# Kernel tuning notes

Measured on AMD Instinct MI355X. Metric: run time of the kernel, lower is better.

Reference implementation:

```python
import jax, jax.numpy as jnp
import numpy as np

B, T, D = 2, 1024, 2048
H, HKV, DH = 16, 4, 128
G = H // HKV  # GQA groups
F = 5632
ROPE_THETA = 10000.0
EPS = 1e-6


def _rope_tables(t, dh, theta):
    inv = 1.0 / (theta ** (np.arange(0, dh, 2, dtype=np.float32) / dh))  # [dh//2]
    ang = np.outer(np.arange(t, dtype=np.float32), inv)                  # [T, dh//2]
    return jnp.asarray(np.cos(ang)), jnp.asarray(np.sin(ang))


def setup_inputs() -> dict:
    key = jax.random.key(0)
    ks = jax.random.split(key, 9)
    s = 0.02
    cos, sin = _rope_tables(T, DH, ROPE_THETA)
    return {
        "x": jax.random.normal(ks[0], (B, T, D), jnp.float32),
        "freqs_cos": cos,
        "freqs_sin": sin,
        "w_norm1": jnp.ones((D,), jnp.float32),
        "w_norm2": jnp.ones((D,), jnp.float32),
        "wq": jax.random.normal(ks[1], (D, H * DH), jnp.float32) * s,
        "wk": jax.random.normal(ks[2], (D, HKV * DH), jnp.float32) * s,
        "wv": jax.random.normal(ks[3], (D, HKV * DH), jnp.float32) * s,
        "wo": jax.random.normal(ks[4], (D, D), jnp.float32) * s,
        "w1": jax.random.normal(ks[5], (D, F), jnp.float32) * s,
        "w2": jax.random.normal(ks[6], (F, D), jnp.float32) * s,
        "w3": jax.random.normal(ks[7], (D, F), jnp.float32) * s,
    }


def _rmsnorm(x, w):
    var = jnp.mean(jnp.square(x), axis=-1, keepdims=True)
    return x * jax.lax.rsqrt(var + EPS) * w


def _apply_rope(x, cos, sin):
    # x: [B, T, nH, DH]; cos/sin: [T, DH//2]
    xr = x.reshape(*x.shape[:-1], DH // 2, 2)
    x0, x1 = xr[..., 0], xr[..., 1]
    c = cos[None, :, None, :]
    s = sin[None, :, None, :]
    o0 = x0 * c - x1 * s
    o1 = x0 * s + x1 * c
    return jnp.stack([o0, o1], axis=-1).reshape(x.shape)


def reference(x, freqs_cos, freqs_sin, w_norm1, w_norm2, wq, wk, wv, wo, w1, w2, w3):
    residual = x
    xn = _rmsnorm(x, w_norm1)
    q = (xn @ wq).reshape(B, T, H, DH)
    k = (xn @ wk).reshape(B, T, HKV, DH)
    v = (xn @ wv).reshape(B, T, HKV, DH)
    q = _apply_rope(q, freqs_cos, freqs_sin)
    k = _apply_rope(k, freqs_cos, freqs_sin)
    # grouped heads: q -> [B, HKV, G, T, DH]; k,v -> [B, HKV, T, DH]
    q = q.transpose(0, 2, 1, 3).reshape(B, HKV, G, T, DH)
    k = k.transpose(0, 2, 1, 3)
    v = v.transpose(0, 2, 1, 3)
    scale = DH ** -0.5
    scores = jnp.einsum("bkgtd,bksd->bkgts", q, k) * scale  # [B,HKV,G,T,T]
    causal = jnp.tril(jnp.ones((T, T), dtype=bool))
    scores = jnp.where(causal, scores, -jnp.inf)
    attn = jax.nn.softmax(scores, axis=-1)
    out = jnp.einsum("bkgts,bksd->bkgtd", attn, v)  # [B,HKV,G,T,DH]
    out = out.reshape(B, H, T, DH).transpose(0, 2, 1, 3).reshape(B, T, D)
    x = residual + out @ wo
    h = _rmsnorm(x, w_norm2)
    ffn = (jax.nn.silu(h @ w1) * (h @ w3)) @ w2
    return x + ffn
```

## Files before the change

kernel.cpp:

```cpp
#include <hip/hip_runtime.h>
#include <hip/hip_bf16.h>
#include <math.h>

typedef __hip_bfloat16 bf16;
typedef __attribute__((ext_vector_type(8))) short bf16x8;
typedef __attribute__((ext_vector_type(4))) float f32x4;

__device__ __forceinline__ float b2f(bf16 v) { return __bfloat162float(v); }
__device__ __forceinline__ bf16  f2b(float v) { return __float2bfloat16(v); }

constexpr int Bc = 2, Tc = 1024, Dc = 2048, Hc = 16, HKVc = 4, DHc = 128, Fc = 5632;
constexpr int Mr = Bc * Tc;
constexpr int Nqkv = Hc * DHc + 2 * HKVc * DHc;

__device__ __forceinline__ void g2l16(void* lds, const void* g) {
  __builtin_amdgcn_global_load_lds(
      (const __attribute__((address_space(1))) unsigned int*)g,
      (__attribute__((address_space(3))) unsigned int*)lds, 16, 0, 0);
}

__global__ __launch_bounds__(256) void tcast_k(const float* __restrict__ src,
                                               bf16* __restrict__ dst,
                                               int N, int K) {
  __shared__ bf16 tile[64][68];
  const int t = threadIdx.x;
  const int n0 = blockIdx.x * 64, k0 = blockIdx.y * 64;
#pragma unroll
  for (int it = 0; it < 4; ++it) {
    const int kl = it * 16 + (t >> 4);
    const int nl = (t & 15) * 4;
    float4 v = *reinterpret_cast<const float4*>(src + (size_t)(k0 + kl) * N + n0 + nl);
    tile[kl][nl]     = f2b(v.x);
    tile[kl][nl + 1] = f2b(v.y);
    tile[kl][nl + 2] = f2b(v.z);
    tile[kl][nl + 3] = f2b(v.w);
  }
  __syncthreads();
  union { uint4 u; bf16 h[8]; } o;
#pragma unroll
  for (int it = 0; it < 2; ++it) {
    const int nl = it * 32 + (t >> 3);
    const int kl = (t & 7) * 8;
#pragma unroll
    for (int j = 0; j < 8; ++j) o.h[j] = tile[kl + j][nl];
    *reinterpret_cast<uint4*>(dst + (size_t)(n0 + nl) * K + k0 + kl) = o.u;
  }
}

__global__ __launch_bounds__(256) void tcast_ffn(const float* __restrict__ src,
                                                 bf16* __restrict__ dst,
                                                 int off) {
  __shared__ bf16 tile[64][68];
  const int t = threadIdx.x;
  const int n0 = blockIdx.x * 64, k0 = blockIdx.y * 64;
#pragma unroll
  for (int it = 0; it < 4; ++it) {
    const int kl = it * 16 + (t >> 4);
    const int nl = (t & 15) * 4;
    float4 v = *reinterpret_cast<const float4*>(src + (size_t)(k0 + kl) * Fc + n0 + nl);
    tile[kl][nl]     = f2b(v.x);
    tile[kl][nl + 1] = f2b(v.y);
    tile[kl][nl + 2] = f2b(v.z);
    tile[kl][nl + 3] = f2b(v.w);
  }
  __syncthreads();
  union { uint4 u; bf16 h[8]; } o;
#pragma unroll
  for (int it = 0; it < 2; ++it) {
    const int nl = it * 32 + (t >> 3);
    const int kl = (t & 7) * 8;
#pragma unroll
    for (int j = 0; j < 8; ++j) o.h[j] = tile[kl + j][nl];
    const int n = n0 + nl;
    const int r = ((n >> 4) << 5) + (n & 15) + off;
    *reinterpret_cast<uint4*>(dst + (size_t)r * Dc + k0 + kl) = o.u;
  }
}

__global__ __launch_bounds__(256) void rmsnorm_k(const float* __restrict__ x,
                                                 const float* __restrict__ w,
                                                 bf16* __restrict__ out) {
  const size_t rbase = (size_t)blockIdx.x * Dc;
  float ss = 0.f;
  for (int i = threadIdx.x; i < Dc; i += 256) {
    float v = x[rbase + i];
    ss += v * v;
  }
#pragma unroll
  for (int off = 32; off > 0; off >>= 1) ss += __shfl_down(ss, off, 64);
  __shared__ float red[4];
  const int lane = threadIdx.x & 63, wid = threadIdx.x >> 6;
  if (lane == 0) red[wid] = ss;
  __syncthreads();
  const float scale = rsqrtf((red[0] + red[1] + red[2] + red[3]) / (float)Dc + 1e-6f);
  for (int i = threadIdx.x; i < Dc; i += 256)
    out[rbase + i] = f2b(x[rbase + i] * scale * w[i]);
}

__global__ __launch_bounds__(256) void reduce4_rms(const float* __restrict__ P,
                                                   const float* __restrict__ x,
                                                   const float* __restrict__ w,
                                                   float* __restrict__ xat,
                                                   bf16* __restrict__ hb) {
  constexpr size_t PS = (size_t)Mr * Dc;
  const size_t base4 = (size_t)blockIdx.x * (Dc / 4);
  const int t = threadIdx.x;
  float4 v[2];
  float ss = 0.f;
#pragma unroll
  for (int j = 0; j < 2; ++j) {
    const size_t c4 = base4 + t + j * 256;
    float4 a = reinterpret_cast<const float4*>(x)[c4];
#pragma unroll
    for (int z = 0; z < 4; ++z) {
      float4 q = reinterpret_cast<const float4*>(P + z * PS)[c4];
      a.x += q.x; a.y += q.y; a.z += q.z; a.w += q.w;
    }
    reinterpret_cast<float4*>(xat)[c4] = a;
    ss += a.x * a.x + a.y * a.y + a.z * a.z + a.w * a.w;
    v[j] = a;
  }
#pragma unroll
  for (int off = 32; off > 0; off >>= 1) ss += __shfl_down(ss, off, 64);
  __shared__ float red[4];
  const int lane = t & 63, wid = t >> 6;
  if (lane == 0) red[wid] = ss;
  __syncthreads();
  const float scale = rsqrtf((red[0] + red[1] + red[2] + red[3]) / (float)Dc + 1e-6f);
  bf16* hrow = hb + (size_t)blockIdx.x * Dc;
#pragma unroll
  for (int j = 0; j < 2; ++j) {
    const int c = (t + j * 256) * 4;
    hrow[c]     = f2b(v[j].x * scale * w[c]);
    hrow[c + 1] = f2b(v[j].y * scale * w[c + 1]);
    hrow[c + 2] = f2b(v[j].z * scale * w[c + 2]);
    hrow[c + 3] = f2b(v[j].w * scale * w[c + 3]);
  }
}

__global__ __launch_bounds__(256) void reduce4_add(const float* __restrict__ P,
                                                   const float* __restrict__ res,
                                                   float* __restrict__ out) {
  constexpr size_t PS = (size_t)Mr * Dc;
  const size_t c4 = (size_t)blockIdx.x * 256 + threadIdx.x;
  float4 a = reinterpret_cast<const float4*>(res)[c4];
#pragma unroll
  for (int z = 0; z < 4; ++z) {
    float4 q = reinterpret_cast<const float4*>(P + z * PS)[c4];
    a.x += q.x; a.y += q.y; a.z += q.z; a.w += q.w;
  }
  reinterpret_cast<float4*>(out)[c4] = a;
}

template <int K>
__global__ __launch_bounds__(512, 2) void ffn_gemm256(const bf16* __restrict__ A,
                                                      const bf16* __restrict__ B,
                                                      bf16* __restrict__ act) {
  constexpr int NT = K / 64;
  constexpr int NIT = NT / 2;
  __shared__ bf16 As[2 * 256 * 64];
  __shared__ bf16 Bs[3 * 256 * 64];
  const int tid = threadIdx.x;
  const int lane = tid & 63, wv = tid >> 6;
  const int wr = wv >> 2, wc = wv & 3;
  const int fr = lane & 15, quad = lane >> 4;
  const int swz = fr & 7;
  const int bm = blockIdx.y * 256;
  const int bn = blockIdx.x * 256;
  const int lrow = tid >> 3;
  const int scol = ((tid & 7) ^ (lrow & 7)) * 8;
  const size_t rstep = (size_t)64 * K;

  auto stageA = [&](int t, int half) {
    const int buf = (t & 1) * 16384;
    const bf16* g = A + (size_t)(bm + half * 128 + lrow) * K + t * 64 + scol;
    bf16* d = As + buf + half * 8192 + (size_t)tid * 8;
    g2l16(d, g);
    g2l16(d + 4096, g + rstep);
  };
  auto stageB = [&](int t, int half, int buf) {
    const bf16* g = B + (size_t)(bn + half * 128 + lrow) * K + t * 64 + scol;
    bf16* d = Bs + buf * 16384 + half * 8192 + (size_t)tid * 8;
    g2l16(d, g);
    g2l16(d + 4096, g + rstep);
  };

  f32x4 acc[8][4] = {};
  const int u0 = (quad ^ swz) * 8;

  stageA(0, 0); stageA(0, 1);
  stageB(0, 0, 0); stageB(0, 1, 0);
  stageB(1, 0, 1); stageB(1, 1, 1);
  asm volatile("s_waitcnt vmcnt(4)" ::: "memory");
  __builtin_amdgcn_s_barrier();

  int rb0 = 0, rb1 = 1, sb = 2;
  for (int it = 0; it < NIT; ++it) {
    const int t1 = 2 * it + 1;
#pragma unroll
    for (int j = 0; j < 8; ++j) {
      const int bufT = (j < 4) ? 0 : 16384;
      const int bufB = ((j < 4) ? rb0 : rb1) * 16384;
      const int qr4 = ((j & 3) >> 1) * 4, qc2 = ((j & 3) & 1) * 2;
      bf16x8 af[4][2], bv[2][2];
      const bf16* Ab = As + bufT + (size_t)(wr * 128 + fr) * 64;
      const bf16* Bb = Bs + bufB + (size_t)(wc * 64 + fr) * 64;
#pragma unroll
      for (int ii = 0; ii < 4; ++ii) {
        af[ii][0] = *reinterpret_cast<const bf16x8*>(Ab + (qr4 + ii) * 1024 + u0);
        af[ii][1] = *reinterpret_cast<const bf16x8*>(Ab + (qr4 + ii) * 1024 + (u0 ^ 32));
      }
#pragma unroll
      for (int jj = 0; jj < 2; ++jj) {
        bv[jj][0] = *reinterpret_cast<const bf16x8*>(Bb + (qc2 + jj) * 1024 + u0);
        bv[jj][1] = *reinterpret_cast<const bf16x8*>(Bb + (qc2 + jj) * 1024 + (u0 ^ 32));
      }
      if (j == 0)      stageA(t1, 0);
      else if (j == 1) stageA(t1, 1);
      else if (j == 2) { if (2 * it + 2 < NT) stageB(2 * it + 2, 0, sb); }
      else if (j == 3) { if (2 * it + 2 < NT) stageB(2 * it + 2, 1, sb); }
      else if (j == 4) { if (2 * it + 2 < NT) stageA(2 * it + 2, 0); }
      else if (j == 5) { if (2 * it + 2 < NT) stageA(2 * it + 2, 1); }
      else if (j == 6) { if (2 * it + 3 < NT) stageB(2 * it + 3, 0, rb0); }
      else             { if (2 * it + 3 < NT) stageB(2 * it + 3, 1, rb0); }
      __builtin_amdgcn_s_barrier();
      asm volatile("s_waitcnt lgkmcnt(0)" ::: "memory");
      __builtin_amdgcn_sched_barrier(0);
      __builtin_amdgcn_s_setprio(1);
#pragma unroll
      for (int ii = 0; ii < 4; ++ii)
#pragma unroll
        for (int jj = 0; jj < 2; ++jj) {
          acc[qr4 + ii][qc2 + jj] = __builtin_amdgcn_mfma_f32_16x16x32_bf16(
              af[ii][0], bv[jj][0], acc[qr4 + ii][qc2 + jj], 0, 0, 0);
          acc[qr4 + ii][qc2 + jj] = __builtin_amdgcn_mfma_f32_16x16x32_bf16(
              af[ii][1], bv[jj][1], acc[qr4 + ii][qc2 + jj], 0, 0, 0);
        }
      __builtin_amdgcn_s_setprio(0);
      if (j == 3) {
        if (2 * it + 2 < NT) asm volatile("s_waitcnt vmcnt(4)" ::: "memory");
        else                 asm volatile("s_waitcnt vmcnt(0)" ::: "memory");
      } else if (j == 7) {
        if (2 * it + 3 < NT)      asm volatile("s_waitcnt vmcnt(4)" ::: "memory");
        else if (2 * it + 2 < NT) asm volatile("s_waitcnt vmcnt(0)" ::: "memory");
      }
      __builtin_amdgcn_s_barrier();
    }
    const int nrb0 = sb; sb = rb1; rb1 = rb0; rb0 = nrb0;
  }

  const int er = quad * 4, ec = lane & 15;
#pragma unroll
  for (int i = 0; i < 8; ++i) {
    const int row = bm + wr * 128 + i * 16 + er;
#pragma unroll
    for (int jp = 0; jp < 2; ++jp) {
      const f32x4 g = acc[i][2 * jp], u = acc[i][2 * jp + 1];
      const int f = blockIdx.x * 128 + wc * 32 + jp * 16 + ec;
#pragma unroll
      for (int r = 0; r < 4; ++r) {
        const float sg = g[r] / (1.f + __expf(-g[r]));
        act[(size_t)(row + r) * Fc + f] = f2b(sg * u[r]);
      }
    }
  }
}

template <int KFULL, int KSUB>
__global__ __launch_bounds__(512, 2) void gemm256sk(const bf16* __restrict__ A,
                                                    const bf16* __restrict__ Bt,
                                                    float* __restrict__ Part,
                                                    int N) {
  constexpr int NT = KSUB / 64;
  constexpr int NIT = NT / 2;
  __shared__ bf16 As[2 * 256 * 64];
  __shared__ bf16 Bs[3 * 256 * 64];
  const int tid = threadIdx.x;
  const int lane = tid & 63, wv = tid >> 6;
  const int wr = wv >> 2, wc = wv & 3;
  const int fr = lane & 15, quad = lane >> 4;
  const int swz = fr & 7;
  const int bm = blockIdx.y * 256;
  const int bn = blockIdx.x * 256;
  const int kbase = blockIdx.z * KSUB;
  const int lrow = tid >> 3;
  const int scol = ((tid & 7) ^ (lrow & 7)) * 8;
  const size_t rstep = (size_t)64 * KFULL;

  auto stageA = [&](int t, int half) {
    const int buf = (t & 1) * 16384;
    const bf16* g = A + (size_t)(bm + half * 128 + lrow) * KFULL + kbase + t * 64 + scol;
    bf16* d = As + buf + half * 8192 + (size_t)tid * 8;
    g2l16(d, g);
    g2l16(d + 4096, g + rstep);
  };
  auto stageB = [&](int t, int half, int buf) {
    const bf16* g = Bt + (size_t)(bn + half * 128 + lrow) * KFULL + kbase + t * 64 + scol;
    bf16* d = Bs + buf * 16384 + half * 8192 + (size_t)tid * 8;
    g2l16(d, g);
    g2l16(d + 4096, g + rstep);
  };

  f32x4 acc[8][4] = {};
  const int u0 = (quad ^ swz) * 8;

  stageA(0, 0); stageA(0, 1);
  stageB(0, 0, 0); stageB(0, 1, 0);
  stageB(1, 0, 1); stageB(1, 1, 1);
  asm volatile("s_waitcnt vmcnt(4)" ::: "memory");
  __builtin_amdgcn_s_barrier();

  int rb0 = 0, rb1 = 1, sb = 2;
  for (int it = 0; it < NIT; ++it) {
    const int t1 = 2 * it + 1;
#pragma unroll
    for (int j = 0; j < 8; ++j) {
      const int bufT = (j < 4) ? 0 : 16384;
      const int bufB = ((j < 4) ? rb0 : rb1) * 16384;
      const int qr4 = ((j & 3) >> 1) * 4, qc2 = ((j & 3) & 1) * 2;
      bf16x8 af[4][2], bv[2][2];
      const bf16* Ab = As + bufT + (size_t)(wr * 128 + fr) * 64;
      const bf16* Bb = Bs + bufB + (size_t)(wc * 64 + fr) * 64;
#pragma unroll
      for (int ii = 0; ii < 4; ++ii) {
        af[ii][0] = *reinterpret_cast<const bf16x8*>(Ab + (qr4 + ii) * 1024 + u0);
        af[ii][1] = *reinterpret_cast<const bf16x8*>(Ab + (qr4 + ii) * 1024 + (u0 ^ 32));
      }
#pragma unroll
      for (int jj = 0; jj < 2; ++jj) {
        bv[jj][0] = *reinterpret_cast<const bf16x8*>(Bb + (qc2 + jj) * 1024 + u0);
        bv[jj][1] = *reinterpret_cast<const bf16x8*>(Bb + (qc2 + jj) * 1024 + (u0 ^ 32));
      }
      if (j == 0)      stageA(t1, 0);
      else if (j == 1) stageA(t1, 1);
      else if (j == 2) { if (2 * it + 2 < NT) stageB(2 * it + 2, 0, sb); }
      else if (j == 3) { if (2 * it + 2 < NT) stageB(2 * it + 2, 1, sb); }
      else if (j == 4) { if (2 * it + 2 < NT) stageA(2 * it + 2, 0); }
      else if (j == 5) { if (2 * it + 2 < NT) stageA(2 * it + 2, 1); }
      else if (j == 6) { if (2 * it + 3 < NT) stageB(2 * it + 3, 0, rb0); }
      else             { if (2 * it + 3 < NT) stageB(2 * it + 3, 1, rb0); }
      __builtin_amdgcn_s_barrier();
      asm volatile("s_waitcnt lgkmcnt(0)" ::: "memory");
      __builtin_amdgcn_sched_barrier(0);
      __builtin_amdgcn_s_setprio(1);
#pragma unroll
      for (int ii = 0; ii < 4; ++ii)
#pragma unroll
        for (int jj = 0; jj < 2; ++jj) {
          acc[qr4 + ii][qc2 + jj] = __builtin_amdgcn_mfma_f32_16x16x32_bf16(
              af[ii][0], bv[jj][0], acc[qr4 + ii][qc2 + jj], 0, 0, 0);
          acc[qr4 + ii][qc2 + jj] = __builtin_amdgcn_mfma_f32_16x16x32_bf16(
              af[ii][1], bv[jj][1], acc[qr4 + ii][qc2 + jj], 0, 0, 0);
        }
      __builtin_amdgcn_s_setprio(0);
      if (j == 3) {
        if (2 * it + 2 < NT) asm volatile("s_waitcnt vmcnt(4)" ::: "memory");
        else                 asm volatile("s_waitcnt vmcnt(0)" ::: "memory");
      } else if (j == 7) {
        if (2 * it + 3 < NT)      asm volatile("s_waitcnt vmcnt(4)" ::: "memory");
        else if (2 * it + 2 < NT) asm volatile("s_waitcnt vmcnt(0)" ::: "memory");
      }
      __builtin_amdgcn_s_barrier();
    }
    const int nrb0 = sb; sb = rb1; rb1 = rb0; rb0 = nrb0;
  }

  float* P = Part + (size_t)blockIdx.z * ((size_t)Mr * N);
  const int er = quad * 4, ec = lane & 15;
#pragma unroll
  for (int i = 0; i < 8; ++i) {
    const int row = bm + wr * 128 + i * 16 + er;
#pragma unroll
    for (int jc = 0; jc < 4; ++jc) {
      const int col = bn + wc * 64 + jc * 16 + ec;
#pragma unroll
      for (int r = 0; r < 4; ++r)
        P[(size_t)(row + r) * N + col] = acc[i][jc][r];
    }
  }
}

__global__ __launch_bounds__(256) void repack_k(const float* __restrict__ P,
                                                const float* __restrict__ cosb,
                                                const float* __restrict__ sinb,
                                                bf16* __restrict__ Qr,
                                                bf16* __restrict__ Kr,
                                                bf16* __restrict__ Vt) {
  constexpr size_t PS = (size_t)Mr * Nqkv;
  const int bt = blockIdx.x;
  const int b = bt >> 10, tp = bt & (Tc - 1);
  const int t0 = threadIdx.x;
  const float* r0 = P + (size_t)bt * Nqkv;
  const float* r1 = r0 + PS;
#pragma unroll
  for (int k = 0; k < 4; ++k) {
    int p2 = k * 256 + t0;
    int hh = p2 >> 6, i = p2 & 63;
    float c = cosb[tp * 64 + i], sn = sinb[tp * 64 + i];
    float2 v0 = *reinterpret_cast<const float2*>(r0 + hh * 128 + 2 * i);
    float2 v1 = *reinterpret_cast<const float2*>(r1 + hh * 128 + 2 * i);
    float x0 = v0.x + v1.x, x1 = v0.y + v1.y;
    bf16* dst = Qr + ((size_t)(b * Hc + hh) * Tc + tp) * DHc + 2 * i;
    dst[0] = f2b(x0 * c - x1 * sn);
    dst[1] = f2b(x0 * sn + x1 * c);
  }
  {
    int hh = t0 >> 6, i = t0 & 63;
    float c = cosb[tp * 64 + i], sn = sinb[tp * 64 + i];
    float2 v0 = *reinterpret_cast<const float2*>(r0 + 2048 + hh * 128 + 2 * i);
    float2 v1 = *reinterpret_cast<const float2*>(r1 + 2048 + hh * 128 + 2 * i);
    float x0 = v0.x + v1.x, x1 = v0.y + v1.y;
    bf16* dst = Kr + ((size_t)(b * HKVc + hh) * Tc + tp) * DHc + 2 * i;
    dst[0] = f2b(x0 * c - x1 * sn);
    dst[1] = f2b(x0 * sn + x1 * c);
  }
#pragma unroll
  for (int k = 0; k < 2; ++k) {
    int e = k * 256 + t0;
    int kvh = e >> 7, dd = e & 127;
    Vt[((size_t)(b * HKVc + kvh) * DHc + dd) * Tc + tp] = f2b(r0[2560 + e] + r1[2560 + e]);
  }
}

__global__ __launch_bounds__(256) void fattn(const bf16* __restrict__ Qr,
                                             const bf16* __restrict__ Kr,
                                             const bf16* __restrict__ Vt,
                                             bf16* __restrict__ ao) {
  __shared__ __align__(16) bf16 Ks[64 * 136];
  __shared__ __align__(16) bf16 Vts[128 * 72];
  __shared__ __align__(16) bf16 Ps[4][16 * 72];
  const int idx = blockIdx.x;
  const int r = idx & 15;
  const int qt = (r & 1) ? (15 - (r >> 1)) : (r >> 1);
  const int h = (idx >> 4) & 15;
  const int b = idx >> 8;
  const int kv = h >> 2;
  const int t = threadIdx.x, lane = t & 63, wv = t >> 6;
  const int fr = lane & 15, quad = lane >> 4;

  const bf16* Qbase = Qr + ((size_t)(b * Hc + h) * Tc + qt * 64) * DHc;
  const bf16* Kbase = Kr + (size_t)(b * HKVc + kv) * Tc * DHc;
  const bf16* Vbase = Vt + (size_t)(b * HKVc + kv) * DHc * Tc;

  bf16x8 qf[4];
#pragma unroll
  for (int c = 0; c < 4; ++c)
    qf[c] = *reinterpret_cast<const bf16x8*>(Qbase + (size_t)(wv * 16 + fr) * DHc + c * 32 + quad * 8);

  float m[4], l[4];
  f32x4 o[8] = {};
#pragma unroll
  for (int r2 = 0; r2 < 4; ++r2) { m[r2] = -3.0e38f; l[r2] = 0.f; }

  for (int kt = 0; kt <= qt; ++kt) {
    __syncthreads();
    {
      const bf16* src = Kbase + (size_t)kt * 64 * DHc;
#pragma unroll
      for (int i2 = 0; i2 < 4; ++i2) {
        int flat = i2 * 256 + t;
        int row = flat >> 4, c16 = flat & 15;
        uint4 v = *reinterpret_cast<const uint4*>(src + (size_t)row * DHc + c16 * 8);
        *reinterpret_cast<uint4*>(&Ks[row * 136 + c16 * 8]) = v;
      }
#pragma unroll
      for (int i2 = 0; i2 < 4; ++i2) {
        int flat = i2 * 256 + t;
        int row = flat >> 3, c8 = flat & 7;
        uint4 v = *reinterpret_cast<const uint4*>(Vbase + (size_t)row * Tc + kt * 64 + c8 * 8);
        *reinterpret_cast<uint4*>(&Vts[row * 72 + c8 * 8]) = v;
      }
    }
    __syncthreads();
    f32x4 s[4];
#pragma unroll
    for (int cb = 0; cb < 4; ++cb) {
      f32x4 acc = {};
#pragma unroll
      for (int kc = 0; kc < 4; ++kc) {
        bf16x8 kf = *reinterpret_cast<const bf16x8*>(&Ks[(cb * 16 + fr) * 136 + kc * 32 + quad * 8]);
        acc = __builtin_amdgcn_mfma_f32_16x16x32_bf16(qf[kc], kf, acc, 0, 0, 0);
      }
      s[cb] = acc * 0.08838834764831845f;
    }
    if (kt == qt) {
#pragma unroll
      for (int cb = 0; cb < 4; ++cb)
#pragma unroll
        for (int r2 = 0; r2 < 4; ++r2) {
          int key = cb * 16 + fr;
          int qg = wv * 16 + quad * 4 + r2;
          if (key > qg) s[cb][r2] = -3.0e38f;
        }
    }
    float tm[4], ts[4];
#pragma unroll
    for (int r2 = 0; r2 < 4; ++r2)
      tm[r2] = fmaxf(fmaxf(s[0][r2], s[1][r2]), fmaxf(s[2][r2], s[3][r2]));
#pragma unroll
    for (int off = 1; off < 16; off <<= 1)
#pragma unroll
      for (int r2 = 0; r2 < 4; ++r2)
        tm[r2] = fmaxf(tm[r2], __shfl_xor(tm[r2], off, 64));
    float al[4];
#pragma unroll
    for (int r2 = 0; r2 < 4; ++r2) {
      float mn = fmaxf(m[r2], tm[r2]);
      al[r2] = __expf(m[r2] - mn);
      m[r2] = mn;
      ts[r2] = 0.f;
    }
#pragma unroll
    for (int cb = 0; cb < 4; ++cb)
#pragma unroll
      for (int r2 = 0; r2 < 4; ++r2) {
        float e = __expf(s[cb][r2] - m[r2]);
        s[cb][r2] = e;
        ts[r2] += e;
      }
#pragma unroll
    for (int off = 1; off < 16; off <<= 1)
#pragma unroll
      for (int r2 = 0; r2 < 4; ++r2)
        ts[r2] += __shfl_xor(ts[r2], off, 64);
#pragma unroll
    for (int r2 = 0; r2 < 4; ++r2) l[r2] = l[r2] * al[r2] + ts[r2];
#pragma unroll
    for (int db = 0; db < 8; ++db)
#pragma unroll
      for (int r2 = 0; r2 < 4; ++r2) o[db][r2] *= al[r2];
    bf16* pw = Ps[wv];
#pragma unroll
    for (int cb = 0; cb < 4; ++cb)
#pragma unroll
      for (int r2 = 0; r2 < 4; ++r2)
        pw[(quad * 4 + r2) * 72 + cb * 16 + fr] = f2b(s[cb][r2]);
    bf16x8 pa[2];
    pa[0] = *reinterpret_cast<const bf16x8*>(&pw[fr * 72 + quad * 8]);
    pa[1] = *reinterpret_cast<const bf16x8*>(&pw[fr * 72 + 32 + quad * 8]);
#pragma unroll
    for (int db = 0; db < 8; ++db) {
      bf16x8 v0 = *reinterpret_cast<const bf16x8*>(&Vts[(db * 16 + fr) * 72 + quad * 8]);
      bf16x8 v1 = *reinterpret_cast<const bf16x8*>(&Vts[(db * 16 + fr) * 72 + 32 + quad * 8]);
      o[db] = __builtin_amdgcn_mfma_f32_16x16x32_bf16(pa[0], v0, o[db], 0, 0, 0);
      o[db] = __builtin_amdgcn_mfma_f32_16x16x32_bf16(pa[1], v1, o[db], 0, 0, 0);
    }
  }
#pragma unroll
  for (int r2 = 0; r2 < 4; ++r2) {
    float inv = 1.f / l[r2];
    int qg = qt * 64 + wv * 16 + quad * 4 + r2;
    bf16* orow = ao + (size_t)(b * Tc + qg) * Dc + h * DHc;
#pragma unroll
    for (int db = 0; db < 8; ++db)
      orow[db * 16 + fr] = f2b(o[db][r2] * inv);
  }
}

extern "C" void kernel_launch(void* const* d_in, const int* in_sizes, int n_in,
                              void* d_out, int out_size, void* d_ws, size_t ws_size,
                              hipStream_t stream) {
  const float* x    = (const float*)d_in[0];
  const float* fcos = (const float*)d_in[1];
  const float* fsin = (const float*)d_in[2];
  const float* wn1  = (const float*)d_in[3];
  const float* wn2  = (const float*)d_in[4];
  const float* wq   = (const float*)d_in[5];
  const float* wk   = (const float*)d_in[6];
  const float* wv   = (const float*)d_in[7];
  const float* wo   = (const float*)d_in[8];
  const float* w1   = (const float*)d_in[9];
  const float* w2   = (const float*)d_in[10];
  const float* w3   = (const float*)d_in[11];

  char* p = (char*)d_ws;
  bf16* wqkv_t = (bf16*)p;                 p += (size_t)Nqkv * Dc * 2;
  float* xat   = (float*)d_ws;
  bf16* wo_t = (bf16*)p;                   p += (size_t)Dc * Dc * 2;
  bf16* w13t = (bf16*)p;                   p += (size_t)2 * Fc * Dc * 2;
  bf16* w2t  = w13t;
  bf16* xn   = (bf16*)p;                   p += (size_t)Mr * Dc * 2;
  bf16* ao   = (bf16*)p;                   p += (size_t)Mr * Dc * 2;
  bf16* act  = (bf16*)p;                   p += (size_t)Mr * Fc * 2;
  float* Pbuf = (float*)p;                 p += (size_t)4 * Mr * Dc * 4;
  bf16* hb = xn;
  bf16* Qr = act;
  bf16* Kr = act + (size_t)Mr * Hc * DHc;
  bf16* Vtb = Kr + (size_t)Mr * HKVc * DHc;

  const dim3 blk(256);
  tcast_k<<<dim3(32, 32), blk, 0, stream>>>(wq, wqkv_t, 2048, 2048);
  tcast_k<<<dim3(8, 32), blk, 0, stream>>>(wk, wqkv_t + (size_t)2048 * 2048, 512, 2048);
  tcast_k<<<dim3(8, 32), blk, 0, stream>>>(wv, wqkv_t + (size_t)2560 * 2048, 512, 2048);
  tcast_k<<<dim3(32, 32), blk, 0, stream>>>(wo, wo_t, 2048, 2048);
  tcast_ffn<<<dim3(88, 32), blk, 0, stream>>>(w1, w13t, 0);
  tcast_ffn<<<dim3(88, 32), blk, 0, stream>>>(w3, w13t, 16);

  rmsnorm_k<<<Mr, blk, 0, stream>>>(x, wn1, xn);
  gemm256sk<Dc, 1024><<<dim3(Nqkv / 256, Mr / 256, 2), dim3(512), 0, stream>>>(xn, wqkv_t, Pbuf, Nqkv);
  repack_k<<<Mr, blk, 0, stream>>>(Pbuf, fcos, fsin, Qr, Kr, Vtb);
  fattn<<<Bc * Hc * 16, blk, 0, stream>>>(Qr, Kr, Vtb, ao);
  gemm256sk<Dc, 512><<<dim3(Dc / 256, Mr / 256, 4), dim3(512), 0, stream>>>(ao, wo_t, Pbuf, Dc);
  reduce4_rms<<<Mr, blk, 0, stream>>>(Pbuf, x, wn2, xat, hb);
  ffn_gemm256<Dc><<<dim3(2 * Fc / 256, Mr / 256), dim3(512), 0, stream>>>(hb, w13t, act);
  tcast_k<<<dim3(32, 88), blk, 0, stream>>>(w2, w2t, 2048, 5632);
  gemm256sk<Fc, 1408><<<dim3(Dc / 256, Mr / 256, 4), dim3(512), 0, stream>>>(act, w2t, Pbuf, Dc);
  reduce4_add<<<Mr * Dc / 1024, blk, 0, stream>>>(Pbuf, xat, (float*)d_out);
}
```

Baseline: 564.3 us.

## Double-buffer K/V tiles in flash attention with async LDS loads and XOR swizzle

The attention kernel now prefetches the next K and V tiles into a second LDS buffer using global_load_lds while MFMAs run on the current tile. The LDS layout changes from a padded layout to an XOR-swizzled one to avoid bank conflicts, and s_setprio raises wave priority around the MFMA sections. This aims to hide global-load latency and cut one barrier per iteration. In exchange it doubles LDS use for K/V, which may lower occupancy, and it depends on the async loads having landed by the single trailing barrier.

```diff
diff --git a/kernel.cpp b/kernel.cpp
--- a/kernel.cpp
+++ b/kernel.cpp
@@ -426,8 +426,8 @@
                                              const bf16* __restrict__ Kr,
                                              const bf16* __restrict__ Vt,
                                              bf16* __restrict__ ao) {
-  __shared__ __align__(16) bf16 Ks[64 * 136];
-  __shared__ __align__(16) bf16 Vts[128 * 72];
+  __shared__ __align__(16) bf16 Ks[2][64 * 128];
+  __shared__ __align__(16) bf16 Vts[2][128 * 64];
   __shared__ __align__(16) bf16 Ps[4][16 * 72];
   const int idx = blockIdx.x;
   const int r = idx & 15;
@@ -442,6 +442,24 @@
   const bf16* Kbase = Kr + (size_t)(b * HKVc + kv) * Tc * DHc;
   const bf16* Vbase = Vt + (size_t)(b * HKVc + kv) * DHc * Tc;
 
+  auto stageK = [&](int kt, int buf) {
+    const bf16* src = Kbase + (size_t)kt * 64 * DHc;
+#pragma unroll
+    for (int rr = 0; rr < 4; ++rr) {
+      const int row = rr * 16 + (t >> 4);
+      const int cS = (t & 15) ^ (row & 7);
+      g2l16(&Ks[buf][rr * 2048 + t * 8], src + row * DHc + cS * 8);
+    }
+  };
+  auto stageV = [&](int kt, int buf) {
+#pragma unroll
+    for (int rr = 0; rr < 4; ++rr) {
+      const int row = rr * 32 + (t >> 3);
+      const int cS = (t & 7) ^ (row & 7);
+      g2l16(&Vts[buf][rr * 2048 + t * 8], Vbase + (size_t)row * Tc + kt * 64 + cS * 8);
+    }
+  };
+
   bf16x8 qf[4];
 #pragma unroll
   for (int c = 0; c < 4; ++c)
@@ -452,37 +470,28 @@
 #pragma unroll
   for (int r2 = 0; r2 < 4; ++r2) { m[r2] = -3.0e38f; l[r2] = 0.f; }
 
+  stageK(0, 0);
+  stageV(0, 0);
+  __syncthreads();
+  int buf = 0;
+
   for (int kt = 0; kt <= qt; ++kt) {
-    __syncthreads();
-    {
-      const bf16* src = Kbase + (size_t)kt * 64 * DHc;
-#pragma unroll
-      for (int i2 = 0; i2 < 4; ++i2) {
-        int flat = i2 * 256 + t;
-        int row = flat >> 4, c16 = flat & 15;
-        uint4 v = *reinterpret_cast<const uint4*>(src + (size_t)row * DHc + c16 * 8);
-        *reinterpret_cast<uint4*>(&Ks[row * 136 + c16 * 8]) = v;
-      }
-#pragma unroll
-      for (int i2 = 0; i2 < 4; ++i2) {
-        int flat = i2 * 256 + t;
-        int row = flat >> 3, c8 = flat & 7;
-        uint4 v = *reinterpret_cast<const uint4*>(Vbase + (size_t)row * Tc + kt * 64 + c8 * 8);
-        *reinterpret_cast<uint4*>(&Vts[row * 72 + c8 * 8]) = v;
-      }
-    }
-    __syncthreads();
+    if (kt < qt) { stageK(kt + 1, buf ^ 1); stageV(kt + 1, buf ^ 1); }
+    const int sw = fr & 7;
     f32x4 s[4];
+    __builtin_amdgcn_s_setprio(1);
 #pragma unroll
     for (int cb = 0; cb < 4; ++cb) {
       f32x4 acc = {};
 #pragma unroll
       for (int kc = 0; kc < 4; ++kc) {
-        bf16x8 kf = *reinterpret_cast<const bf16x8*>(&Ks[(cb * 16 + fr) * 136 + kc * 32 + quad * 8]);
+        bf16x8 kf = *reinterpret_cast<const bf16x8*>(
+            &Ks[buf][(cb * 16 + fr) * 128 + (((kc << 2) + quad) ^ sw) * 8]);
         acc = __builtin_amdgcn_mfma_f32_16x16x32_bf16(qf[kc], kf, acc, 0, 0, 0);
       }
       s[cb] = acc * 0.08838834764831845f;
     }
+    __builtin_amdgcn_s_setprio(0);
     if (kt == qt) {
 #pragma unroll
       for (int cb = 0; cb < 4; ++cb)
@@ -538,13 +547,19 @@
     bf16x8 pa[2];
     pa[0] = *reinterpret_cast<const bf16x8*>(&pw[fr * 72 + quad * 8]);
     pa[1] = *reinterpret_cast<const bf16x8*>(&pw[fr * 72 + 32 + quad * 8]);
+    __builtin_amdgcn_s_setprio(1);
 #pragma unroll
     for (int db = 0; db < 8; ++db) {
-      bf16x8 v0 = *reinterpret_cast<const bf16x8*>(&Vts[(db * 16 + fr) * 72 + quad * 8]);
-      bf16x8 v1 = *reinterpret_cast<const bf16x8*>(&Vts[(db * 16 + fr) * 72 + 32 + quad * 8]);
+      bf16x8 v0 = *reinterpret_cast<const bf16x8*>(
+          &Vts[buf][(db * 16 + fr) * 64 + (quad ^ sw) * 8]);
+      bf16x8 v1 = *reinterpret_cast<const bf16x8*>(
+          &Vts[buf][(db * 16 + fr) * 64 + ((4 + quad) ^ sw) * 8]);
       o[db] = __builtin_amdgcn_mfma_f32_16x16x32_bf16(pa[0], v0, o[db], 0, 0, 0);
       o[db] = __builtin_amdgcn_mfma_f32_16x16x32_bf16(pa[1], v1, o[db], 0, 0, 0);
     }
+    __builtin_amdgcn_s_setprio(0);
+    __syncthreads();
+    buf ^= 1;
   }
 #pragma unroll
   for (int r2 = 0; r2 < 4; ++r2) {
```

New measurement: 561.0 us. No clear change (-0.6%).
